# Kernel optimization log

Hardware: AMD Instinct MI355X
Metric: run time of the kernel (lower is better)

## Reference

```python
import jax, jax.numpy as jnp
import numpy as np

N = 100000
E = 1600000
N_IN = 512
N_H = 128


def setup_inputs() -> dict:
    key = jax.random.key(0)
    ks = jax.random.split(key, 8)
    x = jax.random.normal(ks[0], (N, N_IN), dtype=jnp.float32)
    src = jax.random.randint(ks[1], (E,), 0, N, dtype=jnp.int32)
    dst = jax.random.randint(ks[2], (E,), 0, N, dtype=jnp.int32)
    perm = jax.random.permutation(ks[3], N).astype(jnp.int32)
    # GraphConv params (in_feats=512 -> out_feats=128), xavier-ish scale
    W = jax.random.normal(ks[4], (N_IN, N_H), dtype=jnp.float32) / np.sqrt(N_IN)
    b = jnp.zeros((N_H,), dtype=jnp.float32)
    alpha = jnp.full((N_H,), 0.25, dtype=jnp.float32)  # PReLU(n_h) init
    mlp_W = jax.random.normal(ks[5], (N_H, N_H), dtype=jnp.float32) / np.sqrt(N_H)
    mlp_b = jnp.zeros((N_H,), dtype=jnp.float32)
    return {"x": x, "src": src, "dst": dst, "perm": perm, "W": W, "b": b,
            "alpha": alpha, "mlp_W": mlp_W, "mlp_b": mlp_b, "batch_train": 0}


def _degree_norm(idx, n):
    deg = jax.ops.segment_sum(jnp.ones_like(idx, dtype=jnp.float32), idx, num_segments=n)
    return jnp.clip(deg, 1.0, None) ** -0.5  # [n]


def _gcn_layer(x, src, dst, W, b, alpha):
    n = x.shape[0]
    norm_out = _degree_norm(src, n)  # src-side out-degree norm
    norm_in = _degree_norm(dst, n)   # dst-side in-degree norm
    # in_feats > out_feats: apply weight first (DGL GraphConv ordering)
    h = x @ W                                  # [N, n_h]
    h = h * norm_out[:, None]
    agg = jax.ops.segment_sum(h[src], dst, num_segments=n)  # SpMM copy_u/sum
    agg = agg * norm_in[:, None] + b
    return jnp.where(agg >= 0, agg, alpha * agg)  # PReLU(n_h)


def reference(x, src, dst, perm, W, b, alpha, mlp_W, mlp_b, batch_train):
    z1 = _gcn_layer(x, src, dst, W, b, alpha)          # clean encoder
    z2 = _gcn_layer(x[perm], src, dst, W, b, alpha)    # corrupted encoder
    z1 = z1 @ mlp_W + mlp_b
    z2 = z2 @ mlp_W + mlp_b
    logit = jnp.concatenate((z1.sum(1), z2.sum(1)), axis=0)  # [2N]
    return logit
```

## Files before the change

kernel.cpp:

```cpp
#include <hip/hip_runtime.h>


typedef __bf16 bf16x8 __attribute__((ext_vector_type(8)));
typedef float f32x4 __attribute__((ext_vector_type(4)));

#define PAD 48
#define NBMAX 256
#define EPB 4096
#define EPT 16

__device__ inline unsigned short f2bf(float f) {
  unsigned u = __float_as_uint(f);
  u += 0x7fffu + ((u >> 16) & 1u);
  return (unsigned short)(u >> 16);
}
__device__ inline float2 bfpair(unsigned u) {
  float2 r;
  r.x = __uint_as_float(u << 16);
  r.y = __uint_as_float(u & 0xffff0000u);
  return r;
}

__device__ __forceinline__ void gld16(const void* g, void* l) {
  __builtin_amdgcn_global_load_lds(
      (const __attribute__((address_space(1))) void*)g,
      (__attribute__((address_space(3))) void*)l, 16, 0, 0);
}

__global__ __launch_bounds__(256) void k_bin(const int* __restrict__ src,
                                             const int* __restrict__ dst,
                                             int* __restrict__ gCntD,
                                             int* __restrict__ gCntS,
                                             int* __restrict__ dstbin,
                                             unsigned short* __restrict__ srcbin,
                                             int E, int NB, int CAP) {
  __shared__ int cntD[NBMAX], cntS[NBMAX], baseD[NBMAX], baseS[NBMAX];
  const int tid = threadIdx.x;
  const int e0 = blockIdx.x * EPB;

  for (int b = tid; b < NBMAX; b += 256) { cntD[b] = 0; cntS[b] = 0; }
  __syncthreads();

  int sv[EPT], dv[EPT], pd[EPT], ps[EPT];
#pragma unroll
  for (int it = 0; it < EPT; ++it) {
    int e = e0 + it * 256 + tid;
    sv[it] = -1;
    if (e < E) {
      int s = src[e];
      int d = dst[e];
      sv[it] = s;
      dv[it] = d;
      pd[it] = atomicAdd(&cntD[d >> 9], 1);
      ps[it] = atomicAdd(&cntS[s >> 9], 1);
    }
  }
  __syncthreads();

  for (int b = tid; b < NB; b += 256) {
    baseD[b] = atomicAdd(&gCntD[b], cntD[b]);
    baseS[b] = atomicAdd(&gCntS[b], cntS[b]);
  }
  __syncthreads();

#pragma unroll
  for (int it = 0; it < EPT; ++it) {
    if (sv[it] >= 0) {
      int s = sv[it], d = dv[it];
      int bd = d >> 9;
      int p = baseD[bd] + pd[it];
      if (p < CAP) dstbin[(size_t)bd * CAP + p] = (s << 9) | (d & 511);
      int bs = s >> 9;
      int q = baseS[bs] + ps[it];
      if (q < CAP) srcbin[(size_t)bs * CAP + q] = (unsigned short)(s & 511);
    }
  }
}

__global__ __launch_bounds__(256) void k_post(const int* __restrict__ gCntD,
                                              const int* __restrict__ dstbin,
                                              const int* __restrict__ gCntS,
                                              const unsigned short* __restrict__ srcbin,
                                              const int* __restrict__ perm,
                                              int* __restrict__ col,
                                              int* __restrict__ deg_d,
                                              float* __restrict__ norm_i,
                                              float* __restrict__ norm_o,
                                              int* __restrict__ inv,
                                              int N, int CAP) {
  __shared__ int cnt[512];
  __shared__ int hist[512];
  const int b = blockIdx.x;
  const int tid = threadIdx.x;
  cnt[tid] = 0; cnt[tid + 256] = 0;
  hist[tid] = 0; hist[tid + 256] = 0;
  __syncthreads();

  int cbD = gCntD[b]; if (cbD > CAP) cbD = CAP;
  const int* binD = dstbin + (size_t)b * CAP;
  for (int i = tid; i < cbD; i += 256) {
    int rec = binD[i];
    int d9 = rec & 511;
    int s = rec >> 9;
    int pos = atomicAdd(&cnt[d9], 1);
    if (pos < PAD) col[((size_t)b * 512 + d9) * PAD + pos] = s;
  }
  int cbS = gCntS[b]; if (cbS > CAP) cbS = CAP;
  const unsigned short* binS = srcbin + (size_t)b * CAP;
  for (int i = tid; i < cbS; i += 256) {
    atomicAdd(&hist[binS[i]], 1);
  }
  __syncthreads();

  for (int t = tid; t < 512; t += 256) {
    int i = b * 512 + t;
    if (i < N) {
      int c = cnt[t];
      deg_d[i] = (c > PAD) ? PAD : c;
      norm_i[i] = rsqrtf((float)((c < 1) ? 1 : c));
      int h = hist[t];
      norm_o[i] = rsqrtf((float)((h < 1) ? 1 : h));
      inv[perm[i]] = i;
    }
  }
}

__global__ __launch_bounds__(256) void k_fill_dev(const int* __restrict__ src,
                                                  const int* __restrict__ dst,
                                                  int* __restrict__ deg_s,
                                                  int* __restrict__ cnt,
                                                  int* __restrict__ col, int E) {
  int t = blockIdx.x * 256 + threadIdx.x;
  int e0 = t * 4;
  if (e0 >= E) return;
  int e1 = (e0 + 4 < E) ? e0 + 4 : E;
  for (int e = e0; e < e1; e++) {
    int s = src[e], d = dst[e];
    atomicAdd(&deg_s[s], 1);
    int pos = atomicAdd(&cnt[d], 1);
    if (pos < PAD) col[(size_t)d * PAD + pos] = s;
  }
}

__global__ __launch_bounds__(256) void k_finish_dev(const int* __restrict__ deg_s,
                                                    const int* __restrict__ cnt,
                                                    const int* __restrict__ perm,
                                                    float* __restrict__ norm_o,
                                                    float* __restrict__ norm_i,
                                                    int* __restrict__ deg_d,
                                                    int* __restrict__ inv, int N) {
  int i = blockIdx.x * 256 + threadIdx.x;
  if (i >= N) return;
  int a = deg_s[i]; if (a < 1) a = 1;
  int b = cnt[i];
  deg_d[i] = (b > PAD) ? PAD : b;
  if (b < 1) b = 1;
  norm_o[i] = rsqrtf((float)a);
  norm_i[i] = rsqrtf((float)b);
  inv[perm[i]] = i;
}

__global__ __launch_bounds__(256) void k_castw(const float* __restrict__ W,
                                               unsigned short* __restrict__ WT) {
  int i = blockIdx.x * 256 + threadIdx.x;
  int k = i >> 7;
  int n = i & 127;
  WT[n * 512 + k] = f2bf(W[i]);
}

__global__ __launch_bounds__(256) void k_gemm(const float* __restrict__ X,
                                              const unsigned short* __restrict__ WT,
                                              const float* __restrict__ norm_o,
                                              const int* __restrict__ inv,
                                              unsigned short* __restrict__ HH, int M) {
  __shared__ __align__(16) unsigned short Bs[2][128 * 64];
  unsigned short* smem = &Bs[0][0];

  const int tid = threadIdx.x;
  const int wave = tid >> 6;
  const int lane = tid & 63;
  const int m = lane & 15;
  const int quad = lane >> 4;
  const int block_row = blockIdx.x * 64;

  int arow = block_row + wave * 16 + m;
  if (arow >= M) arow = M - 1;
  const float* xrow = X + (size_t)arow * 512 + quad * 8;

  const unsigned short* srcB[4];
  int dstB[4];
#pragma unroll
  for (int u = 0; u < 4; ++u) {
    int L = tid + u * 256;
    int n = L >> 3;
    int s = L & 7;
    int sp = s ^ (n & 7);
    srcB[u] = WT + (size_t)n * 512 + sp * 8;
    dstB[u] = n * 64 + s * 8;
  }

  f32x4 acc[8];
#pragma unroll
  for (int t = 0; t < 8; t++) acc[t] = (f32x4){0.f, 0.f, 0.f, 0.f};

  auto stageB = [&](int buf, int c) {
    const int k0 = c * 64;
#pragma unroll
    for (int u = 0; u < 4; ++u) gld16(srcB[u] + k0, &Bs[buf][dstB[u]]);
  };

  stageB(0, 0);
  f32x4 a0 = *(const f32x4*)(xrow);
  f32x4 a1 = *(const f32x4*)(xrow + 4);
  __syncthreads();

  int cur = 0;
#pragma unroll
  for (int c = 0; c < 8; ++c) {
    if (c < 7) stageB(cur ^ 1, c + 1);
#pragma unroll
    for (int st = 0; st < 2; ++st) {
      const int ks = c * 2 + st;
      f32x4 na0 = (f32x4){0.f, 0.f, 0.f, 0.f};
      f32x4 na1 = (f32x4){0.f, 0.f, 0.f, 0.f};
      if (ks < 15) {
        na0 = *(const f32x4*)(xrow + (ks + 1) * 32);
        na1 = *(const f32x4*)(xrow + (ks + 1) * 32 + 4);
      }
      union { bf16x8 v; __bf16 h[8]; } au;
#pragma unroll
      for (int j = 0; j < 4; ++j) {
        au.h[j] = (__bf16)a0[j];
        au.h[4 + j] = (__bf16)a1[j];
      }
      const int q = st * 4 + quad;
#pragma unroll
      for (int t = 0; t < 8; ++t) {
        int R = t * 16 + m;
        bf16x8 b = *(const bf16x8*)&Bs[cur][R * 64 + ((q ^ (R & 7)) * 8)];
        acc[t] = __builtin_amdgcn_mfma_f32_16x16x32_bf16(au.v, b, acc[t], 0, 0, 0);
      }
      a0 = na0;
      a1 = na1;
    }
    __syncthreads();
    cur ^= 1;
  }

  float no1[4], no2[4];
#pragma unroll
  for (int rr4 = 0; rr4 < 4; rr4++) {
    int rr = block_row + wave * 16 + quad * 4 + rr4;
    no1[rr4] = 0.f;
    no2[rr4] = 0.f;
    if (rr < M) {
      no1[rr4] = norm_o[rr];
      no2[rr4] = norm_o[inv[rr]];
    }
  }

#pragma unroll
  for (int t = 0; t < 8; t++) {
    int c = t * 16 + m;
#pragma unroll
    for (int rr4 = 0; rr4 < 4; rr4++) {
      int row = wave * 16 + quad * 4 + rr4;
      smem[row * 128 + c] = f2bf(acc[t][rr4] * no1[rr4]);
    }
  }
  __syncthreads();
#pragma unroll
  for (int it = 0; it < 4; it++) {
    int idx = tid + it * 256;
    int row = idx >> 4;
    int c8 = (idx & 15) * 8;
    int gr = block_row + row;
    if (gr < M)
      *(int4*)(HH + (size_t)gr * 256 + c8) = *(int4*)&smem[row * 128 + c8];
  }
  __syncthreads();

#pragma unroll
  for (int t = 0; t < 8; t++) {
    int c = t * 16 + m;
#pragma unroll
    for (int rr4 = 0; rr4 < 4; rr4++) {
      int row = wave * 16 + quad * 4 + rr4;
      smem[row * 128 + c] = f2bf(acc[t][rr4] * no2[rr4]);
    }
  }
  __syncthreads();
#pragma unroll
  for (int it = 0; it < 4; it++) {
    int idx = tid + it * 256;
    int row = idx >> 4;
    int c8 = (idx & 15) * 8;
    int gr = block_row + row;
    if (gr < M) {
      int q = inv[gr];
      *(int4*)(HH + (size_t)q * 256 + 128 + c8) = *(int4*)&smem[row * 128 + c8];
    }
  }
}

__global__ __launch_bounds__(128) void k_wsum(const float* __restrict__ mlpW,
                                              const float* __restrict__ mlpb,
                                              float* __restrict__ wsum,
                                              float* __restrict__ bsum) {
  __shared__ float sb[128];
  int k = threadIdx.x;
  float s = 0.f;
  for (int j = 0; j < 128; j++) s += mlpW[k * 128 + j];
  wsum[k] = s;
  sb[k] = mlpb[k];
  __syncthreads();
  for (int off = 64; off > 0; off >>= 1) {
    if (k < off) sb[k] += sb[k + off];
    __syncthreads();
  }
  if (k == 0) bsum[0] = sb[0];
}

__global__ __launch_bounds__(256) void k_agg(const unsigned short* __restrict__ HH,
                                             const int* __restrict__ deg_d,
                                             const int* __restrict__ col,
                                             const float* __restrict__ norm_i,
                                             const float* __restrict__ bias,
                                             const float* __restrict__ alpha,
                                             const float* __restrict__ wsum,
                                             const float* __restrict__ bsum,
                                             float* __restrict__ out, int N) {
  int wave = (blockIdx.x * 256 + threadIdx.x) >> 6;
  int lane = threadIdx.x & 63;
  if (wave >= N) return;
  const int g = lane >> 4;
  const int sl = lane & 15;

  int cl = deg_d[wave];
  const int* cbase = col + (size_t)wave * PAD;

  float a1[8], a2[8];
#pragma unroll
  for (int i = 0; i < 8; i++) { a1[i] = 0.f; a2[i] = 0.f; }

  for (int j0 = 0; j0 < cl; j0 += 16) {
    int4 r1[4], r2[4];
    float mk[4];
#pragma unroll
    for (int u = 0; u < 4; ++u) {
      int j = j0 + u * 4 + g;
      int je = (j < cl) ? j : cl - 1;
      int s = cbase[je];
      mk[u] = (j < cl) ? 1.f : 0.f;
      const unsigned short* rp = HH + (size_t)s * 256 + sl * 8;
      r1[u] = *(const int4*)rp;
      r2[u] = *(const int4*)(rp + 128);
    }
#pragma unroll
    for (int u = 0; u < 4; ++u) {
      const unsigned* u1 = (const unsigned*)&r1[u];
      const unsigned* u2 = (const unsigned*)&r2[u];
#pragma unroll
      for (int q = 0; q < 4; q++) {
        float2 v1 = bfpair(u1[q]);
        float2 v2 = bfpair(u2[q]);
        a1[2 * q]     = fmaf(v1.x, mk[u], a1[2 * q]);
        a1[2 * q + 1] = fmaf(v1.y, mk[u], a1[2 * q + 1]);
        a2[2 * q]     = fmaf(v2.x, mk[u], a2[2 * q]);
        a2[2 * q + 1] = fmaf(v2.y, mk[u], a2[2 * q + 1]);
      }
    }
  }

#pragma unroll
  for (int i = 0; i < 8; i++) {
    a1[i] += __shfl_xor(a1[i], 16);
    a1[i] += __shfl_xor(a1[i], 32);
    a2[i] += __shfl_xor(a2[i], 16);
    a2[i] += __shfl_xor(a2[i], 32);
  }

  float ni = norm_i[wave];
  float4 bb0 = ((const float4*)bias)[sl * 2];
  float4 bb1 = ((const float4*)bias)[sl * 2 + 1];
  float4 al0 = ((const float4*)alpha)[sl * 2];
  float4 al1 = ((const float4*)alpha)[sl * 2 + 1];
  float4 ws0 = ((const float4*)wsum)[sl * 2];
  float4 ws1 = ((const float4*)wsum)[sl * 2 + 1];
  float bs = bsum[0];
  float bb[8] = {bb0.x, bb0.y, bb0.z, bb0.w, bb1.x, bb1.y, bb1.z, bb1.w};
  float al[8] = {al0.x, al0.y, al0.z, al0.w, al1.x, al1.y, al1.z, al1.w};
  float wsv[8] = {ws0.x, ws0.y, ws0.z, ws0.w, ws1.x, ws1.y, ws1.z, ws1.w};

  float p1 = 0.f, p2 = 0.f;
#pragma unroll
  for (int i = 0; i < 8; i++) {
    float g1 = a1[i] * ni + bb[i];
    float g2 = a2[i] * ni + bb[i];
    g1 = (g1 >= 0.f) ? g1 : al[i] * g1;
    g2 = (g2 >= 0.f) ? g2 : al[i] * g2;
    p1 = fmaf(g1, wsv[i], p1);
    p2 = fmaf(g2, wsv[i], p2);
  }
#pragma unroll
  for (int off = 8; off > 0; off >>= 1) {
    p1 += __shfl_down(p1, off);
    p2 += __shfl_down(p2, off);
  }
  if (lane == 0) {
    out[wave] = p1 + bs;
    out[N + wave] = p2 + bs;
  }
}


extern "C" void kernel_launch(void* const* d_in, const int* in_sizes, int n_in,
                              void* d_out, int out_size, void* d_ws, size_t ws_size,
                              hipStream_t stream) {
  const float* x = (const float*)d_in[0];
  const int* src = (const int*)d_in[1];
  const int* dst = (const int*)d_in[2];
  const int* perm = (const int*)d_in[3];
  const float* W = (const float*)d_in[4];
  const float* bias = (const float*)d_in[5];
  const float* alpha = (const float*)d_in[6];
  const float* mlpW = (const float*)d_in[7];
  const float* mlpb = (const float*)d_in[8];

  const int E = in_sizes[1];
  const int N = in_sizes[3];
  float* out = (float*)d_out;

  char* ws = (char*)d_ws;
  size_t off = 0;
  auto alloc = [&](size_t bytes) -> void* {
    void* p = ws + off;
    off = (off + bytes + 255) & ~(size_t)255;
    return p;
  };

  unsigned short* HH = (unsigned short*)alloc((size_t)N * 256 * sizeof(unsigned short));
  int* col = (int*)alloc((size_t)N * PAD * sizeof(int));
  unsigned short* WT = (unsigned short*)alloc(512 * 128 * sizeof(unsigned short));
  float* norm_o = (float*)alloc((size_t)N * sizeof(float));
  float* norm_i = (float*)alloc((size_t)N * sizeof(float));
  int* inv = (int*)alloc((size_t)N * sizeof(int));
  int* deg_d = (int*)alloc((size_t)N * sizeof(int));
  float* wsum = (float*)alloc(512);
  float* bsum = (float*)alloc(256);
  size_t common = off;

  const int NB = (N + 511) >> 9;
  const int meanB = (NB > 0) ? E / NB : 0;
  const int CAP = ((meanB * 5) / 4 + 1023) & ~1023;

  size_t need_binned = common + (size_t)NB * CAP * sizeof(int) +
                       (size_t)NB * CAP * sizeof(unsigned short) +
                       2 * (size_t)NBMAX * sizeof(int) + 4096;
  bool binned = (NB <= NBMAX) && ((ws_size == 0) || (ws_size >= need_binned));

  const int nbN = (N + 255) / 256;
  const int nbE4 = ((E + 3) / 4 + 255) / 256;

  k_castw<<<512 * 128 / 256, 256, 0, stream>>>(W, WT);
  k_wsum<<<1, 128, 0, stream>>>(mlpW, mlpb, wsum, bsum);

  if (binned) {
    int* dstbin = (int*)alloc((size_t)NB * CAP * sizeof(int));
    unsigned short* srcbin = (unsigned short*)alloc((size_t)NB * CAP * sizeof(unsigned short));
    int* gCntD = (int*)alloc((size_t)NBMAX * sizeof(int));
    int* gCntS = (int*)alloc((size_t)NBMAX * sizeof(int));
    hipMemsetAsync(gCntD, 0, (size_t)NBMAX * sizeof(int), stream);
    hipMemsetAsync(gCntS, 0, (size_t)NBMAX * sizeof(int), stream);
    const int nbBin = (E + EPB - 1) / EPB;
    k_bin<<<nbBin, 256, 0, stream>>>(src, dst, gCntD, gCntS, dstbin, srcbin,
                                     E, NB, CAP);
    k_post<<<NB, 256, 0, stream>>>(gCntD, dstbin, gCntS, srcbin, perm, col,
                                   deg_d, norm_i, norm_o, inv, N, CAP);
  } else {
    int* deg_s = (int*)alloc((size_t)N * sizeof(int));
    int* cnt = (int*)alloc((size_t)N * sizeof(int));
    hipMemsetAsync(deg_s, 0, (size_t)N * sizeof(int), stream);
    hipMemsetAsync(cnt, 0, (size_t)N * sizeof(int), stream);
    k_fill_dev<<<nbE4, 256, 0, stream>>>(src, dst, deg_s, cnt, col, E);
    k_finish_dev<<<nbN, 256, 0, stream>>>(deg_s, cnt, perm, norm_o, norm_i,
                                          deg_d, inv, N);
  }

  k_gemm<<<(N + 63) / 64, 256, 0, stream>>>(x, WT, norm_o, inv, HH, N);
  k_agg<<<(N + 3) / 4, 256, 0, stream>>>(HH, deg_d, col, norm_i,
                                         bias, alpha, wsum, bsum, out, N);
}
```

Measured before the change: 510.5 us.

## Stage binned edges in LDS and write bins out with coalesced stores

The binning kernel now does a block-wide prefix scan over per-bin counts and scatters edge records into shared memory sorted by bin. It then writes them out contiguously, using a binary search over the bin offsets to find each element's destination. Consecutive threads therefore write consecutive addresses within a bin instead of scattering randomly to global memory. The cost is extra LDS usage (about 24KB more per block), extra barriers, and a per-element binary search. The code also assumes NB ≤ 256 because it indexes by tid.

```diff
diff --git a/kernel.cpp b/kernel.cpp
--- a/kernel.cpp
+++ b/kernel.cpp
@@ -34,11 +34,17 @@
                                              int* __restrict__ dstbin,
                                              unsigned short* __restrict__ srcbin,
                                              int E, int NB, int CAP) {
-  __shared__ int cntD[NBMAX], cntS[NBMAX], baseD[NBMAX], baseS[NBMAX];
+  __shared__ int cntD[NBMAX], cntS[NBMAX];
+  __shared__ int offD[NBMAX], offS[NBMAX];
+  __shared__ int baseD[NBMAX], baseS[NBMAX];
+  __shared__ int recD[EPB];
+  __shared__ unsigned short recS[EPB];
   const int tid = threadIdx.x;
   const int e0 = blockIdx.x * EPB;
-
-  for (int b = tid; b < NBMAX; b += 256) { cntD[b] = 0; cntS[b] = 0; }
+  const int nloc = min(EPB, E - e0);
+
+  cntD[tid] = 0;
+  cntS[tid] = 0;
   __syncthreads();
 
   int sv[EPT], dv[EPT], pd[EPT], ps[EPT];
@@ -57,9 +63,27 @@
   }
   __syncthreads();
 
-  for (int b = tid; b < NB; b += 256) {
-    baseD[b] = atomicAdd(&gCntD[b], cntD[b]);
-    baseS[b] = atomicAdd(&gCntS[b], cntS[b]);
+  const int vD = cntD[tid];
+  const int vS = cntS[tid];
+  offD[tid] = vD;
+  offS[tid] = vS;
+  __syncthreads();
+  for (int sh = 1; sh < 256; sh <<= 1) {
+    int aD = (tid >= sh) ? offD[tid - sh] : 0;
+    int aS = (tid >= sh) ? offS[tid - sh] : 0;
+    __syncthreads();
+    offD[tid] += aD;
+    offS[tid] += aS;
+    __syncthreads();
+  }
+  int exD = offD[tid] - vD;
+  int exS = offS[tid] - vS;
+  __syncthreads();
+  offD[tid] = exD;
+  offS[tid] = exS;
+  if (tid < NB) {
+    baseD[tid] = atomicAdd(&gCntD[tid], vD);
+    baseS[tid] = atomicAdd(&gCntS[tid], vS);
   }
   __syncthreads();
 
@@ -67,13 +91,28 @@
   for (int it = 0; it < EPT; ++it) {
     if (sv[it] >= 0) {
       int s = sv[it], d = dv[it];
-      int bd = d >> 9;
-      int p = baseD[bd] + pd[it];
-      if (p < CAP) dstbin[(size_t)bd * CAP + p] = (s << 9) | (d & 511);
-      int bs = s >> 9;
-      int q = baseS[bs] + ps[it];
-      if (q < CAP) srcbin[(size_t)bs * CAP + q] = (unsigned short)(s & 511);
-    }
+      recD[offD[d >> 9] + pd[it]] = (s << 9) | (d & 511);
+      recS[offS[s >> 9] + ps[it]] = (unsigned short)(s & 511);
+    }
+  }
+  __syncthreads();
+
+  for (int i = tid; i < nloc; i += 256) {
+    int lo = 0, hi = NB - 1;
+    while (lo < hi) {
+      int mid = (lo + hi + 1) >> 1;
+      if (offD[mid] <= i) lo = mid; else hi = mid - 1;
+    }
+    int p = baseD[lo] + (i - offD[lo]);
+    if (p < CAP) dstbin[(size_t)lo * CAP + p] = recD[i];
+
+    lo = 0; hi = NB - 1;
+    while (lo < hi) {
+      int mid = (lo + hi + 1) >> 1;
+      if (offS[mid] <= i) lo = mid; else hi = mid - 1;
+    }
+    int q = baseS[lo] + (i - offS[lo]);
+    if (q < CAP) srcbin[(size_t)lo * CAP + q] = recS[i];
   }
 }
 
```

Measured after the change: 521.4 us. 1.02x slower.
